# Kernel tuning notes

Hardware: AMD Instinct MI355X
Metric: run time of the kernel (lower is better)

The kernel has to match this reference:

```python
import jax, jax.numpy as jnp
import numpy as np

N = 50000          # num member nodes == num provider nodes
E = 800000         # provider->member bipartite edges (avg degree 16)
IN_M = 128; IN_P = 128; HID = 128; HEADS = 4; LAT = 64
NEG = 0.2          # leaky_relu negative slope (PyG GATConv default)


def gat_conv(x, src, dst, W, a_src, a_dst, b, heads, ch):
    """PyG-style GATConv (eval mode, concat heads). x:[N,F], src/dst:[Etot]."""
    n = x.shape[0]
    h = (x @ W).reshape(n, heads, ch)                       # [N,H,C]
    s = jnp.sum(h * a_src, axis=-1)                         # [N,H]
    d = jnp.sum(h * a_dst, axis=-1)                         # [N,H]
    e = jax.nn.leaky_relu(s[src] + d[dst], NEG)             # [Etot,H]
    # segment softmax over edges grouped by destination node
    m = jax.ops.segment_max(e, dst, num_segments=n)
    p = jnp.exp(e - m[dst])
    z = jax.ops.segment_sum(p, dst, num_segments=n)
    alpha = p / (z[dst] + 1e-16)                            # [Etot,H]
    out = jax.ops.segment_sum(h[src] * alpha[..., None], dst, num_segments=n)
    return out.reshape(n, heads * ch) + b


def setup_inputs() -> dict:
    key = jax.random.key(0)
    ks = jax.random.split(key, 24)
    gl = lambda k, shape, fan: (jax.random.normal(k, shape, jnp.float32) / np.sqrt(fan).astype(np.float32))
    return {
        "x_member": jax.random.normal(ks[0], (N, IN_M), jnp.float32),
        "x_provider": jax.random.normal(ks[1], (N, IN_P), jnp.float32),
        "edge_index": jax.random.randint(ks[2], (2, E), 0, N),
        "W1_m": gl(ks[3], (IN_M, HID), IN_M),
        "a_src1_m": gl(ks[4], (HEADS, HID // HEADS), HID // HEADS),
        "a_dst1_m": gl(ks[5], (HEADS, HID // HEADS), HID // HEADS),
        "b1_m": jnp.zeros((HID,), jnp.float32),
        "W2_m": gl(ks[6], (HID, LAT), HID),
        "a_src2_m": gl(ks[7], (1, LAT), LAT),
        "a_dst2_m": gl(ks[8], (1, LAT), LAT),
        "b2_m": jnp.zeros((LAT,), jnp.float32),
        "W1_p": gl(ks[9], (IN_P, HID), IN_P),
        "a_src1_p": gl(ks[10], (HEADS, HID // HEADS), HID // HEADS),
        "a_dst1_p": gl(ks[11], (HEADS, HID // HEADS), HID // HEADS),
        "b1_p": jnp.zeros((HID,), jnp.float32),
        "W2_p": gl(ks[12], (HID, LAT), HID),
        "a_src2_p": gl(ks[13], (1, LAT), LAT),
        "a_dst2_p": gl(ks[14], (1, LAT), LAT),
        "b2_p": jnp.zeros((LAT,), jnp.float32),
        "Wd_m": gl(ks[15], (LAT, IN_M), LAT),
        "bd_m": jnp.zeros((IN_M,), jnp.float32),
        "Wd_p": gl(ks[16], (LAT, IN_P), LAT),
        "bd_p": jnp.zeros((IN_P,), jnp.float32),
    }


def reference(x_member, x_provider, edge_index,
              W1_m, a_src1_m, a_dst1_m, b1_m, W2_m, a_src2_m, a_dst2_m, b2_m,
              W1_p, a_src1_p, a_dst1_p, b1_p, W2_p, a_src2_p, a_dst2_p, b2_p,
              Wd_m, bd_m, Wd_p, bd_p):
    prov, memb = edge_index[0], edge_index[1]
    loop = jnp.arange(N)
    # member graph: self loops + (provider -> member); provider graph: reverse
    m_src = jnp.concatenate([loop, prov]); m_dst = jnp.concatenate([loop, memb])
    p_src = jnp.concatenate([loop, memb]); p_dst = jnp.concatenate([loop, prov])

    xm = jax.nn.elu(gat_conv(x_member, m_src, m_dst, W1_m, a_src1_m, a_dst1_m, b1_m, HEADS, HID // HEADS))
    z_m = gat_conv(xm, m_src, m_dst, W2_m, a_src2_m, a_dst2_m, b2_m, 1, LAT)

    xp = jax.nn.elu(gat_conv(x_provider, p_src, p_dst, W1_p, a_src1_p, a_dst1_p, b1_p, HEADS, HID // HEADS))
    z_p = gat_conv(xp, p_src, p_dst, W2_p, a_src2_p, a_dst2_p, b2_p, 1, LAT)

    x_hat_member = z_m @ Wd_m + bd_m
    x_hat_provider = z_p @ Wd_p + bd_p
    edge_logits = jnp.sum(z_p[prov] * z_m[memb], axis=1)
    return (x_hat_member, x_hat_provider, edge_logits)
```

## Files before the change

kernel.cpp:

```cpp
#include <hip/hip_runtime.h>
#include <hip/hip_fp16.h>
#include <stdint.h>

__device__ __forceinline__ unsigned int pack_h2(float a, float b) {
    return (unsigned int)__half_as_ushort(__float2half(a)) |
           ((unsigned int)__half_as_ushort(__float2half(b)) << 16);
}
__device__ __forceinline__ float4 cvt_h4(uint2 r) {
    __half2 h0 = *reinterpret_cast<__half2*>(&r.x);
    __half2 h1 = *reinterpret_cast<__half2*>(&r.y);
    float2 f0 = __half22float2(h0), f1 = __half22float2(h1);
    return make_float4(f0.x, f0.y, f1.x, f1.y);
}

template<int K, int COUT, bool ADD_BIAS, bool IN_HALF, bool OUT_HALF, int SDH>
__global__ __launch_bounds__(256) void gemm_kernel(const void* __restrict__ X0,
                                                   const void* __restrict__ X1,
                                                   const float* __restrict__ W0,
                                                   const float* __restrict__ W1,
                                                   const float* __restrict__ b0,
                                                   const float* __restrict__ b1,
                                                   const float* __restrict__ as0,
                                                   const float* __restrict__ ad0,
                                                   const float* __restrict__ as1,
                                                   const float* __restrict__ ad1,
                                                   float* __restrict__ s_out,
                                                   float* __restrict__ d_out,
                                                   void* __restrict__ out0,
                                                   void* __restrict__ out1, int n)
{
    constexpr int KC   = 64;
    constexpr int CPT  = (COUT >= 128) ? 8 : 4;
    constexpr int TX   = COUT / CPT;
    constexpr int TY   = 256 / TX;
    constexpr int ROWS = TY * 4;

    __shared__ float Wl[KC * COUT];
    __shared__ float Xl[KC * ROWS];

    const int side = blockIdx.y;
    const void*  Xv   = side ? X1 : X0;
    const float* W    = side ? W1 : W0;
    const float* bias = side ? b1 : b0;
    void* outp        = side ? out1 : out0;

    const int tid  = threadIdx.x;
    const int row0 = blockIdx.x * ROWS;
    const int tx = tid % TX, ty = tid / TX;
    const int c0 = tx * CPT;

    float acc[4][CPT];
    #pragma unroll
    for (int i = 0; i < 4; ++i)
        #pragma unroll
        for (int j = 0; j < CPT; ++j) acc[i][j] = 0.f;

    for (int k0 = 0; k0 < K; k0 += KC) {
        for (int i = tid; i < KC * COUT / 4; i += 256) {
            int e0 = i * 4;
            int r = e0 / COUT, c = e0 - r * COUT;
            reinterpret_cast<float4*>(Wl)[i] =
                *reinterpret_cast<const float4*>(W + (size_t)(k0 + r) * COUT + c);
        }
        for (int i = tid; i < ROWS * KC / 4; i += 256) {
            int r = i / (KC / 4), c4 = i - r * (KC / 4);
            int gr = row0 + r;
            float4 v = make_float4(0.f, 0.f, 0.f, 0.f);
            if (gr < n) {
                if constexpr (IN_HALF) {
                    const __half* X = (const __half*)Xv;
                    v = cvt_h4(*reinterpret_cast<const uint2*>(X + (size_t)gr * K + k0 + c4 * 4));
                } else {
                    const float* X = (const float*)Xv;
                    v = *reinterpret_cast<const float4*>(X + (size_t)gr * K + k0 + c4 * 4);
                }
            }
            int cb = c4 * 4;
            Xl[(cb + 0) * ROWS + r] = v.x;
            Xl[(cb + 1) * ROWS + r] = v.y;
            Xl[(cb + 2) * ROWS + r] = v.z;
            Xl[(cb + 3) * ROWS + r] = v.w;
        }
        __syncthreads();

        #pragma unroll 16
        for (int kk = 0; kk < KC; ++kk) {
            float b[CPT];
            #pragma unroll
            for (int j = 0; j < CPT; ++j) b[j] = Wl[kk * COUT + c0 + j];
            float4 a4 = *reinterpret_cast<const float4*>(Xl + kk * ROWS + ty * 4);
            float a[4] = {a4.x, a4.y, a4.z, a4.w};
            #pragma unroll
            for (int i = 0; i < 4; ++i)
                #pragma unroll
                for (int j = 0; j < CPT; ++j)
                    acc[i][j] = fmaf(a[i], b[j], acc[i][j]);
        }
        __syncthreads();
    }

    float ascr[CPT], adtr[CPT];
    int hd = 0;
    if constexpr (SDH > 0) {
        constexpr int CHh = COUT / SDH;
        hd = c0 / CHh;
        const float* asc = (side ? as1 : as0) + c0;
        const float* adt = (side ? ad1 : ad0) + c0;
        #pragma unroll
        for (int j = 0; j < CPT; ++j) { ascr[j] = asc[j]; adtr[j] = adt[j]; }
    }

    #pragma unroll
    for (int i = 0; i < 4; ++i) {
        int gr = row0 + ty * 4 + i;
        if (gr < n) {
            float v[CPT];
            #pragma unroll
            for (int j = 0; j < CPT; ++j) {
                v[j] = acc[i][j];
                if constexpr (ADD_BIAS) v[j] += bias[c0 + j];
            }
            if constexpr (SDH > 0) {
                constexpr int CHh = COUT / SDH;
                constexpr int GL = CHh / CPT;
                float ps = 0.f, pd = 0.f;
                #pragma unroll
                for (int j = 0; j < CPT; ++j) {
                    ps = fmaf(v[j], ascr[j], ps);
                    pd = fmaf(v[j], adtr[j], pd);
                }
                #pragma unroll
                for (int o = 1; o < GL; o <<= 1) {
                    ps += __shfl_xor(ps, o, 64);
                    pd += __shfl_xor(pd, o, 64);
                }
                if ((tx % GL) == 0) {
                    size_t gi = (size_t)(side ? n + gr : gr) * SDH + hd;
                    s_out[gi] = ps; d_out[gi] = pd;
                }
            }
            if constexpr (OUT_HALF) {
                __half* po = (__half*)outp + (size_t)gr * COUT + c0;
                if constexpr (CPT == 8) {
                    uint4 w;
                    w.x = pack_h2(v[0], v[1]); w.y = pack_h2(v[2], v[3]);
                    w.z = pack_h2(v[4], v[5]); w.w = pack_h2(v[6], v[7]);
                    *reinterpret_cast<uint4*>(po) = w;
                } else {
                    uint2 w;
                    w.x = pack_h2(v[0], v[1]); w.y = pack_h2(v[2], v[3]);
                    *reinterpret_cast<uint2*>(po) = w;
                }
            } else {
                float* po = (float*)outp + (size_t)gr * COUT + c0;
                #pragma unroll
                for (int j = 0; j < CPT; ++j) po[j] = v[j];
            }
        }
    }
}

#define BSH 7
#define BCAP 2560
#define CHUNK_E 4096

__global__ __launch_bounds__(256) void bucket_scatter_kernel(const int* __restrict__ prov,
                                                             const int* __restrict__ memb,
                                                             int* __restrict__ bcnt,
                                                             int2* __restrict__ bstore,
                                                             int e, int n, int nbuck)
{
    __shared__ int hist[1024];
    __shared__ int lbase[1024];
    const int tid = threadIdx.x;
    const int e0 = blockIdx.x * CHUNK_E;
    const int e1 = min(e, e0 + CHUNK_E);

    for (int i = tid; i < nbuck; i += 256) hist[i] = 0;
    __syncthreads();
    for (int t = e0 + tid; t < e1; t += 256) {
        int m = memb[t], p = prov[t];
        atomicAdd(&hist[m >> BSH], 1);
        atomicAdd(&hist[(n + p) >> BSH], 1);
    }
    __syncthreads();
    for (int i = tid; i < nbuck; i += 256) {
        int h = hist[i];
        lbase[i] = (h > 0) ? atomicAdd(&bcnt[i], h) : 0;
        hist[i] = 0;
    }
    __syncthreads();
    for (int t = e0 + tid; t < e1; t += 256) {
        int m = memb[t], p = prov[t];
        int b1 = m >> BSH;
        int pos1 = lbase[b1] + atomicAdd(&hist[b1], 1);
        if (pos1 < BCAP) bstore[(size_t)b1 * BCAP + pos1] = make_int2(m, p);
        int d2 = n + p;
        int b2 = d2 >> BSH;
        int pos2 = lbase[b2] + atomicAdd(&hist[b2], 1);
        if (pos2 < BCAP) bstore[(size_t)b2 * BCAP + pos2] = make_int2(d2, m);
    }
}

__global__ __launch_bounds__(1024) void bucket_scan_kernel(const int* __restrict__ bcnt,
                                                           int* __restrict__ bbase,
                                                           int* __restrict__ roff,
                                                           int nb, int n2)
{
    __shared__ int tmp[1024];
    int tid = threadIdx.x;
    int v = (tid < nb) ? min(bcnt[tid], BCAP) : 0;
    tmp[tid] = v; __syncthreads();
    for (int o = 1; o < 1024; o <<= 1) {
        int x = (tid >= o) ? tmp[tid - o] : 0;
        __syncthreads();
        tmp[tid] += x;
        __syncthreads();
    }
    bbase[tid] = tmp[tid] - v;
    if (tid == 0) roff[n2] = tmp[1023];
}

__global__ __launch_bounds__(256) void bucket_build_kernel(const int* __restrict__ bcnt,
                                                           const int* __restrict__ bbase,
                                                           const int2* __restrict__ bstore,
                                                           int* __restrict__ roff,
                                                           int* __restrict__ colA,
                                                           int n2)
{
    __shared__ int2 ent[BCAP];
    __shared__ int  colL[BCAP];
    __shared__ int  cnts[128], pref[128], curs[128];

    const int b = blockIdx.x, tid = threadIdx.x;
    const int node0 = b << BSH;
    const int cnt  = min(bcnt[b], BCAP);
    const int base = bbase[b];

    if (tid < 128) cnts[tid] = 0;
    __syncthreads();
    for (int i = tid; i < cnt; i += 256) {
        int2 v = bstore[(size_t)b * BCAP + i];
        ent[i] = v;
        atomicAdd(&cnts[v.x - node0], 1);
    }
    __syncthreads();
    if (tid < 128) pref[tid] = cnts[tid];
    __syncthreads();
    #pragma unroll
    for (int o = 1; o < 128; o <<= 1) {
        int x = 0;
        if (tid < 128 && tid >= o) x = pref[tid - o];
        __syncthreads();
        if (tid < 128) pref[tid] += x;
        __syncthreads();
    }
    if (tid < 128) {
        int node = node0 + tid;
        if (node < n2) roff[node] = base + pref[tid] - cnts[tid];
        curs[tid] = 0;
    }
    __syncthreads();
    for (int i = tid; i < cnt; i += 256) {
        int2 v = ent[i];
        int loc = v.x - node0;
        int slot = (pref[loc] - cnts[loc]) + atomicAdd(&curs[loc], 1);
        colL[slot] = v.y;
    }
    __syncthreads();
    for (int i = tid; i < cnt; i += 256) colA[base + i] = colL[i];
}

template<int H>
__device__ __forceinline__ void store_alpha(__half* __restrict__ A, size_t e, const float* a) {
    if constexpr (H == 4) {
        uint2 w; w.x = pack_h2(a[0], a[1]); w.y = pack_h2(a[2], a[3]);
        *reinterpret_cast<uint2*>(A + e * 4) = w;
    } else {
        A[e] = __float2half(a[0]);
    }
}

template<int H>
__device__ __forceinline__ void alpha_one_fullwave(int iG, int lane,
                                                   const float* __restrict__ sarr,
                                                   const float* __restrict__ sb,
                                                   const float* __restrict__ darr,
                                                   const int* __restrict__ roff,
                                                   const int* __restrict__ col,
                                                   __half* __restrict__ A,
                                                   __half* __restrict__ aselfA)
{
    const int start = roff[iG], end = roff[iG + 1];
    const int deg = end - start;

    float dh[H], es[H];
    #pragma unroll
    for (int hh = 0; hh < H; ++hh) {
        dh[hh] = darr[(size_t)iG * H + hh];
        float e = sarr[(size_t)iG * H + hh] + dh[hh];
        es[hh] = fmaxf(e, 0.2f * e);
    }

    if (deg <= 64) {
        int srcL = (lane < deg) ? col[start + lane] : 0;
        float pl[H];
        if (lane < deg) {
            #pragma unroll
            for (int hh = 0; hh < H; ++hh) {
                float e = sb[(size_t)srcL * H + hh] + dh[hh];
                pl[hh] = __expf(fmaxf(e, 0.2f * e));
            }
        } else {
            #pragma unroll
            for (int hh = 0; hh < H; ++hh) pl[hh] = 0.f;
        }
        float zh[H];
        #pragma unroll
        for (int hh = 0; hh < H; ++hh) zh[hh] = pl[hh];
        #pragma unroll
        for (int hh = 0; hh < H; ++hh)
            for (int o = 32; o >= 1; o >>= 1)
                zh[hh] += __shfl_xor(zh[hh], o, 64);
        float av[H], sf[H];
        #pragma unroll
        for (int hh = 0; hh < H; ++hh) {
            float se = __expf(es[hh]);
            float invz = 1.f / (zh[hh] + se + 1e-16f);
            sf[hh] = se * invz;
            av[hh] = pl[hh] * invz;
        }
        if (lane < deg) store_alpha<H>(A, (size_t)(start + lane), av);
        if (lane == 0) store_alpha<H>(aselfA, (size_t)iG, sf);
        return;
    }

    float zh[H];
    #pragma unroll
    for (int hh = 0; hh < H; ++hh) zh[hh] = 0.f;
    for (int base = start; base < end; base += 64) {
        int idx = base + lane;
        if (idx < end) {
            int src = col[idx];
            #pragma unroll
            for (int hh = 0; hh < H; ++hh) {
                float e = sb[(size_t)src * H + hh] + dh[hh];
                e = fmaxf(e, 0.2f * e);
                zh[hh] += __expf(e);
            }
        }
    }
    #pragma unroll
    for (int hh = 0; hh < H; ++hh)
        for (int o = 32; o >= 1; o >>= 1)
            zh[hh] += __shfl_xor(zh[hh], o, 64);
    float invz[H], sf[H];
    #pragma unroll
    for (int hh = 0; hh < H; ++hh) {
        float se = __expf(es[hh]);
        invz[hh] = 1.f / (zh[hh] + se + 1e-16f);
        sf[hh] = se * invz[hh];
    }
    if (lane == 0) store_alpha<H>(aselfA, (size_t)iG, sf);
    for (int base = start; base < end; base += 64) {
        int idx = base + lane;
        if (idx < end) {
            int src = col[idx];
            float av[H];
            #pragma unroll
            for (int hh = 0; hh < H; ++hh) {
                float e = sb[(size_t)src * H + hh] + dh[hh];
                e = fmaxf(e, 0.2f * e);
                av[hh] = __expf(e) * invz[hh];
            }
            store_alpha<H>(A, (size_t)idx, av);
        }
    }
}

template<int H>
__global__ __launch_bounds__(256) void alpha_kernel(const float* __restrict__ sarr,
                                                    const float* __restrict__ darr,
                                                    const int* __restrict__ roff,
                                                    const int* __restrict__ col,
                                                    __half* __restrict__ A,
                                                    __half* __restrict__ aselfA, int N)
{
    const int n2 = 2 * N;
    const int lane = threadIdx.x & 63;
    const int g = lane >> 5, l = lane & 31;
    const int nw  = (gridDim.x * 256) >> 6;
    const int wv0 = (blockIdx.x * 256 + threadIdx.x) >> 6;
    const int npair = (n2 + 1) >> 1;

    for (int pr = wv0; pr < npair; pr += nw) {
        const int i0 = pr * 2;
        const bool nval = (i0 + g) < n2;
        const int iN = nval ? (i0 + g) : (n2 - 1);
        const int start = roff[iN], end = roff[iN + 1];
        const int deg = nval ? (end - start) : 0;
        const int degO = __shfl_xor(deg, 32, 64);

        if (max(deg, degO) <= 32) {
            const int side = (iN >= N) ? 1 : 0;
            const float* sb = sarr + (size_t)side * N * H;
            float dh[H], es[H];
            if constexpr (H == 4) {
                float4 dv = *reinterpret_cast<const float4*>(darr + (size_t)iN * 4);
                float4 sv = *reinterpret_cast<const float4*>(sarr + (size_t)iN * 4);
                dh[0] = dv.x; dh[1] = dv.y; dh[2] = dv.z; dh[3] = dv.w;
                float ev[4] = {sv.x + dv.x, sv.y + dv.y, sv.z + dv.z, sv.w + dv.w};
                #pragma unroll
                for (int hh = 0; hh < 4; ++hh) es[hh] = fmaxf(ev[hh], 0.2f * ev[hh]);
            } else {
                #pragma unroll
                for (int hh = 0; hh < H; ++hh) {
                    dh[hh] = darr[(size_t)iN * H + hh];
                    float e = sarr[(size_t)iN * H + hh] + dh[hh];
                    es[hh] = fmaxf(e, 0.2f * e);
                }
            }
            int srcL = (l < deg) ? col[start + l] : 0;
            float pl[H];
            if (l < deg) {
                if constexpr (H == 4) {
                    float4 sv = *reinterpret_cast<const float4*>(sb + (size_t)srcL * 4);
                    float ee[4] = {sv.x + dh[0], sv.y + dh[1], sv.z + dh[2], sv.w + dh[3]};
                    #pragma unroll
                    for (int hh = 0; hh < 4; ++hh) pl[hh] = __expf(fmaxf(ee[hh], 0.2f * ee[hh]));
                } else {
                    #pragma unroll
                    for (int hh = 0; hh < H; ++hh) {
                        float e = sb[(size_t)srcL * H + hh] + dh[hh];
                        pl[hh] = __expf(fmaxf(e, 0.2f * e));
                    }
                }
            } else {
                #pragma unroll
                for (int hh = 0; hh < H; ++hh) pl[hh] = 0.f;
            }
            float zh[H];
            #pragma unroll
            for (int hh = 0; hh < H; ++hh) zh[hh] = pl[hh];
            #pragma unroll
            for (int hh = 0; hh < H; ++hh)
                #pragma unroll
                for (int o = 16; o >= 1; o >>= 1)
                    zh[hh] += __shfl_xor(zh[hh], o, 64);
            float av[H], sf[H];
            #pragma unroll
            for (int hh = 0; hh < H; ++hh) {
                float se = __expf(es[hh]);
                float invz = 1.f / (zh[hh] + se + 1e-16f);
                sf[hh] = se * invz;
                av[hh] = pl[hh] * invz;
            }
            if (l < deg) store_alpha<H>(A, (size_t)(start + l), av);
            if (l == 0 && nval) store_alpha<H>(aselfA, (size_t)iN, sf);
        } else {
            for (int nd = 0; nd < 2; ++nd) {
                int i = i0 + nd;
                if (i >= n2) break;
                int sd2 = (i >= N) ? 1 : 0;
                alpha_one_fullwave<H>(i, lane, sarr, sarr + (size_t)sd2 * N * H, darr,
                                      roff, col, A, aselfA);
            }
        }
    }
}

template<int C, int H, bool ELU, bool OUTH>
__global__ __launch_bounds__(256) void gather_kernel(const __half* __restrict__ hm,
                                                     const __half* __restrict__ hp,
                                                     const __half* __restrict__ A,
                                                     const __half* __restrict__ aselfA,
                                                     const int* __restrict__ roff,
                                                     const int* __restrict__ col,
                                                     const float* __restrict__ bias_m,
                                                     const float* __restrict__ bias_p,
                                                     void* __restrict__ out_m,
                                                     void* __restrict__ out_p, int N)
{
    constexpr int CH  = C / H;
    constexpr int LRd = C / 8;
    constexpr int EPd = 32 / LRd;
    const int n2 = 2 * N;
    const int lane = threadIdx.x & 63;
    const int g = lane >> 5, l = lane & 31;
    const int sub = l / LRd, q = l % LRd;
    const int c0 = q * 8;
    const int hd = c0 / CH;
    const int nw  = (gridDim.x * 256) >> 6;
    const int wv0 = (blockIdx.x * 256 + threadIdx.x) >> 6;
    const int npair = (n2 + 1) >> 1;

    for (int pr = wv0; pr < npair; pr += nw) {
        const int i0 = pr * 2;
        const bool nval = (i0 + g) < n2;
        const int iN = nval ? (i0 + g) : (n2 - 1);
        const int side = (iN >= N) ? 1 : 0;
        const int lN = iN - side * N;
        const __half* hf = side ? hp : hm;
        const int start = roff[iN];
        const int deg = roff[iN + 1] - start;

        float acc[8];
        #pragma unroll
        for (int j = 0; j < 8; ++j) acc[j] = 0.f;
        if (sub == 0) {
            uint4 r = *reinterpret_cast<const uint4*>(hf + (size_t)lN * C + c0);
            float4 lo = cvt_h4(make_uint2(r.x, r.y));
            float4 hi = cvt_h4(make_uint2(r.z, r.w));
            float a = __half2float(aselfA[(size_t)iN * H + hd]);
            acc[0] = a * lo.x; acc[1] = a * lo.y; acc[2] = a * lo.z; acc[3] = a * lo.w;
            acc[4] = a * hi.x; acc[5] = a * hi.y; acc[6] = a * hi.z; acc[7] = a * hi.w;
        }
        int t = sub;
#define GSTEP(U)                                                                     \
        while (t + (U - 1) * EPd < deg) {                                            \
            int ss[U]; float aa[U]; uint4 rr[U];                                     \
            _Pragma("unroll")                                                        \
            for (int u = 0; u < U; ++u) {                                            \
                int e = start + t + u * EPd;                                         \
                ss[u] = col[e];                                                      \
                aa[u] = __half2float(A[(size_t)e * H + hd]);                         \
            }                                                                        \
            _Pragma("unroll")                                                        \
            for (int u = 0; u < U; ++u)                                              \
                rr[u] = *reinterpret_cast<const uint4*>(hf + (size_t)ss[u] * C + c0); \
            _Pragma("unroll")                                                        \
            for (int u = 0; u < U; ++u) {                                            \
                float4 lo = cvt_h4(make_uint2(rr[u].x, rr[u].y));                    \
                float4 hi = cvt_h4(make_uint2(rr[u].z, rr[u].w));                    \
                acc[0] = fmaf(aa[u], lo.x, acc[0]);                                  \
                acc[1] = fmaf(aa[u], lo.y, acc[1]);                                  \
                acc[2] = fmaf(aa[u], lo.z, acc[2]);                                  \
                acc[3] = fmaf(aa[u], lo.w, acc[3]);                                  \
                acc[4] = fmaf(aa[u], hi.x, acc[4]);                                  \
                acc[5] = fmaf(aa[u], hi.y, acc[5]);                                  \
                acc[6] = fmaf(aa[u], hi.z, acc[6]);                                  \
                acc[7] = fmaf(aa[u], hi.w, acc[7]);                                  \
            }                                                                        \
            t += U * EPd;                                                            \
        }
        GSTEP(4)
        GSTEP(2)
        GSTEP(1)
#undef GSTEP
        #pragma unroll
        for (int o = LRd; o < 32; o <<= 1) {
            #pragma unroll
            for (int j = 0; j < 8; ++j) acc[j] += __shfl_xor(acc[j], o, 64);
        }
        if (sub == 0 && nval) {
            const float* biasS = side ? bias_p : bias_m;
            float4 b0 = *reinterpret_cast<const float4*>(biasS + c0);
            float4 b1 = *reinterpret_cast<const float4*>(biasS + c0 + 4);
            float v[8] = {acc[0] + b0.x, acc[1] + b0.y, acc[2] + b0.z, acc[3] + b0.w,
                          acc[4] + b1.x, acc[5] + b1.y, acc[6] + b1.z, acc[7] + b1.w};
            if constexpr (ELU) {
                #pragma unroll
                for (int j = 0; j < 8; ++j) v[j] = (v[j] > 0.f) ? v[j] : (__expf(v[j]) - 1.f);
            }
            if constexpr (OUTH) {
                __half* outS = (__half*)(side ? out_p : out_m);
                uint4 w;
                w.x = pack_h2(v[0], v[1]); w.y = pack_h2(v[2], v[3]);
                w.z = pack_h2(v[4], v[5]); w.w = pack_h2(v[6], v[7]);
                *reinterpret_cast<uint4*>(outS + (size_t)lN * C + c0) = w;
            } else {
                float* outS = (float*)(side ? out_p : out_m);
                float* po = outS + (size_t)lN * C + c0;
                *reinterpret_cast<float4*>(po)     = make_float4(v[0], v[1], v[2], v[3]);
                *reinterpret_cast<float4*>(po + 4) = make_float4(v[4], v[5], v[6], v[7]);
            }
        }
    }
}

__global__ __launch_bounds__(256) void logits_kernel(const __half* __restrict__ zp,
                                                     const __half* __restrict__ zm,
                                                     const int* __restrict__ prov,
                                                     const int* __restrict__ memb,
                                                     float* __restrict__ outv, int e)
{
    const int nw   = (gridDim.x * 256) >> 6;
    const int wv   = (blockIdx.x * 256 + threadIdx.x) >> 6;
    const int lane = threadIdx.x & 63;
    const int g = lane >> 3, q = lane & 7;
    const int c0 = q * 8;
    for (int base = wv * 16; base < e; base += nw * 16) {
        int e1 = base + g, e2 = base + 8 + g;
        bool v1 = e1 < e, v2 = e2 < e;
        int i1 = v1 ? e1 : (e - 1), i2 = v2 ? e2 : (e - 1);
        int p1 = prov[i1], m1 = memb[i1];
        int p2 = prov[i2], m2 = memb[i2];
        uint4 a1 = *reinterpret_cast<const uint4*>(zp + (size_t)p1 * 64 + c0);
        uint4 b1 = *reinterpret_cast<const uint4*>(zm + (size_t)m1 * 64 + c0);
        uint4 a2 = *reinterpret_cast<const uint4*>(zp + (size_t)p2 * 64 + c0);
        uint4 b2 = *reinterpret_cast<const uint4*>(zm + (size_t)m2 * 64 + c0);
        float4 al1 = cvt_h4(make_uint2(a1.x, a1.y)), ah1 = cvt_h4(make_uint2(a1.z, a1.w));
        float4 bl1 = cvt_h4(make_uint2(b1.x, b1.y)), bh1 = cvt_h4(make_uint2(b1.z, b1.w));
        float4 al2 = cvt_h4(make_uint2(a2.x, a2.y)), ah2 = cvt_h4(make_uint2(a2.z, a2.w));
        float4 bl2 = cvt_h4(make_uint2(b2.x, b2.y)), bh2 = cvt_h4(make_uint2(b2.z, b2.w));
        float s1 = al1.x * bl1.x + al1.y * bl1.y + al1.z * bl1.z + al1.w * bl1.w
                 + ah1.x * bh1.x + ah1.y * bh1.y + ah1.z * bh1.z + ah1.w * bh1.w;
        float s2 = al2.x * bl2.x + al2.y * bl2.y + al2.z * bl2.z + al2.w * bl2.w
                 + ah2.x * bh2.x + ah2.y * bh2.y + ah2.z * bh2.z + ah2.w * bh2.w;
        #pragma unroll
        for (int o = 1; o < 8; o <<= 1) {
            s1 += __shfl_xor(s1, o, 64);
            s2 += __shfl_xor(s2, o, 64);
        }
        if (q == 0) {
            if (v1) outv[e1] = s1;
            if (v2) outv[e2] = s2;
        }
    }
}

extern "C" void kernel_launch(void* const* d_in, const int* in_sizes, int n_in,
                              void* d_out, int out_size, void* d_ws, size_t ws_size,
                              hipStream_t stream)
{
    const int N_ = in_sizes[0] / 128;
    const int E_ = in_sizes[2] / 2;

    const float* x_member   = (const float*)d_in[0];
    const float* x_provider = (const float*)d_in[1];
    const int*   prov = (const int*)d_in[2];
    const int*   memb = prov + E_;
    const float* W1_m = (const float*)d_in[3];
    const float* a_src1_m = (const float*)d_in[4];
    const float* a_dst1_m = (const float*)d_in[5];
    const float* b1_m = (const float*)d_in[6];
    const float* W2_m = (const float*)d_in[7];
    const float* a_src2_m = (const float*)d_in[8];
    const float* a_dst2_m = (const float*)d_in[9];
    const float* b2_m = (const float*)d_in[10];
    const float* W1_p = (const float*)d_in[11];
    const float* a_src1_p = (const float*)d_in[12];
    const float* a_dst1_p = (const float*)d_in[13];
    const float* b1_p = (const float*)d_in[14];
    const float* W2_p = (const float*)d_in[15];
    const float* a_src2_p = (const float*)d_in[16];
    const float* a_dst2_p = (const float*)d_in[17];
    const float* b2_p = (const float*)d_in[18];
    const float* Wd_m = (const float*)d_in[19];
    const float* bd_m = (const float*)d_in[20];
    const float* Wd_p = (const float*)d_in[21];
    const float* bd_p = (const float*)d_in[22];

    const int n2 = 2 * N_;
    const int NB = (n2 + 127) >> BSH;

    char* p = (char*)d_ws;
    auto alloc = [&](size_t bytes) { void* q = (void*)p; p += (bytes + 255) & ~(size_t)255; return q; };
    __half* h1m   = (__half*)alloc((size_t)N_ * 128 * 2);
    __half* h1p   = (__half*)alloc((size_t)N_ * 128 * 2);
    __half* xm16m = (__half*)alloc((size_t)N_ * 128 * 2);
    __half* xm16p = (__half*)alloc((size_t)N_ * 128 * 2);
    __half* zm16  = (__half*)alloc((size_t)N_ * 64 * 2);
    __half* zp16  = (__half*)alloc((size_t)N_ * 64 * 2);
    float* s1     = (float*)alloc((size_t)n2 * 4 * 4);
    float* d1     = (float*)alloc((size_t)n2 * 4 * 4);
    __half* alpha2= (__half*)alloc((size_t)2 * E_ * 2);
    __half* aselfH= (__half*)alloc((size_t)n2 * 4 * 2);
    int*   bcnt   = (int*)alloc((size_t)NB * 4);
    int*   bbase  = (int*)alloc(1024 * 4);
    int*   roff2  = (int*)alloc((size_t)(n2 + 1) * 4);
    int*   colA   = (int*)alloc((size_t)2 * E_ * 4);
    __half* h2m = h1m;
    __half* h2p = h1p;
    int2*  bstore = (int2*)h1m;
    __half* alpha1 = zm16;

    hipMemsetAsync(bcnt, 0, (size_t)NB * 4, stream);
    bucket_scatter_kernel<<<(E_ + CHUNK_E - 1) / CHUNK_E, 256, 0, stream>>>(prov, memb, bcnt, bstore, E_, N_, NB);
    bucket_scan_kernel<<<1, 1024, 0, stream>>>(bcnt, bbase, roff2, NB, n2);
    bucket_build_kernel<<<NB, 256, 0, stream>>>(bcnt, bbase, bstore, roff2, colA, n2);

    const dim3 gg((N_ + 63) / 64, 2);
    float* out = (float*)d_out;

    gemm_kernel<128, 128, false, false, true, 4><<<gg, 256, 0, stream>>>(
        x_member, x_provider, W1_m, W1_p, nullptr, nullptr,
        a_src1_m, a_dst1_m, a_src1_p, a_dst1_p, s1, d1, h1m, h1p, N_);
    alpha_kernel<4><<<2048, 256, 0, stream>>>(s1, d1, roff2, colA, alpha1, aselfH, N_);
    gather_kernel<128, 4, true, true><<<2048, 256, 0, stream>>>(
        h1m, h1p, alpha1, aselfH, roff2, colA, b1_m, b1_p, xm16m, xm16p, N_);

    gemm_kernel<128, 64, false, true, true, 1><<<gg, 256, 0, stream>>>(
        xm16m, xm16p, W2_m, W2_p, nullptr, nullptr,
        a_src2_m, a_dst2_m, a_src2_p, a_dst2_p, s1, d1, h2m, h2p, N_);
    alpha_kernel<1><<<2048, 256, 0, stream>>>(s1, d1, roff2, colA, alpha2, aselfH, N_);
    gather_kernel<64, 1, false, true><<<2048, 256, 0, stream>>>(
        h2m, h2p, alpha2, aselfH, roff2, colA, b2_m, b2_p, zm16, zp16, N_);

    gemm_kernel<64, 128, true, true, false, 0><<<gg, 256, 0, stream>>>(
        zm16, zp16, Wd_m, Wd_p, bd_m, bd_p,
        nullptr, nullptr, nullptr, nullptr, nullptr, nullptr,
        out, out + (size_t)N_ * 128, N_);
    logits_kernel<<<2048, 256, 0, stream>>>(zp16, zm16, prov, memb, out + (size_t)N_ * 128 * 2, E_);
}
```

Measured before the change: 474.3 us.

## Restructure GEMM shared-memory layout to avoid bank conflicts and interleave column groups

Rewrites the dense GEMM tile so each thread owns two interleaved 4-column groups, 64 columns apart, instead of 8 contiguous columns. The X tile stride is padded by one to reduce LDS bank conflicts on the transposed stores. The K chunk is halved to 32 and the load loops are unrolled. The attention-score reduction is rewritten per head layout to match the new column mapping. The padded stride stops the A reads from being float4-aligned, so they become scalar LDS loads. Smaller K chunks also double the number of syncs.

```diff
diff --git a/kernel.cpp b/kernel.cpp
--- a/kernel.cpp
+++ b/kernel.cpp
@@ -29,14 +29,15 @@
                                                    void* __restrict__ out0,
                                                    void* __restrict__ out1, int n)
 {
-    constexpr int KC   = 64;
-    constexpr int CPT  = (COUT >= 128) ? 8 : 4;
-    constexpr int TX   = COUT / CPT;
+    constexpr int KC   = 32;
+    constexpr int NG   = (COUT >= 128) ? 2 : 1;
+    constexpr int TX   = COUT / (4 * NG);
     constexpr int TY   = 256 / TX;
     constexpr int ROWS = TY * 4;
+    constexpr int XS   = ROWS + 1;
 
     __shared__ float Wl[KC * COUT];
-    __shared__ float Xl[KC * ROWS];
+    __shared__ float Xl[KC * XS];
 
     const int side = blockIdx.y;
     const void*  Xv   = side ? X1 : X0;
@@ -47,21 +48,24 @@
     const int tid  = threadIdx.x;
     const int row0 = blockIdx.x * ROWS;
     const int tx = tid % TX, ty = tid / TX;
-    const int c0 = tx * CPT;
-
-    float acc[4][CPT];
+
+    float acc[4][NG][4];
     #pragma unroll
     for (int i = 0; i < 4; ++i)
         #pragma unroll
-        for (int j = 0; j < CPT; ++j) acc[i][j] = 0.f;
+        for (int g = 0; g < NG; ++g)
+            #pragma unroll
+            for (int j = 0; j < 4; ++j) acc[i][g][j] = 0.f;
 
     for (int k0 = 0; k0 < K; k0 += KC) {
+        #pragma unroll
         for (int i = tid; i < KC * COUT / 4; i += 256) {
             int e0 = i * 4;
             int r = e0 / COUT, c = e0 - r * COUT;
             reinterpret_cast<float4*>(Wl)[i] =
                 *reinterpret_cast<const float4*>(W + (size_t)(k0 + r) * COUT + c);
         }
+        #pragma unroll
         for (int i = tid; i < ROWS * KC / 4; i += 256) {
             int r = i / (KC / 4), c4 = i - r * (KC / 4);
             int gr = row0 + r;
@@ -76,85 +80,112 @@
                 }
             }
             int cb = c4 * 4;
-            Xl[(cb + 0) * ROWS + r] = v.x;
-            Xl[(cb + 1) * ROWS + r] = v.y;
-            Xl[(cb + 2) * ROWS + r] = v.z;
-            Xl[(cb + 3) * ROWS + r] = v.w;
+            Xl[(cb + 0) * XS + r] = v.x;
+            Xl[(cb + 1) * XS + r] = v.y;
+            Xl[(cb + 2) * XS + r] = v.z;
+            Xl[(cb + 3) * XS + r] = v.w;
         }
         __syncthreads();
 
         #pragma unroll 16
         for (int kk = 0; kk < KC; ++kk) {
-            float b[CPT];
-            #pragma unroll
-            for (int j = 0; j < CPT; ++j) b[j] = Wl[kk * COUT + c0 + j];
-            float4 a4 = *reinterpret_cast<const float4*>(Xl + kk * ROWS + ty * 4);
-            float a[4] = {a4.x, a4.y, a4.z, a4.w};
+            float4 b[NG];
+            #pragma unroll
+            for (int g = 0; g < NG; ++g)
+                b[g] = *reinterpret_cast<const float4*>(Wl + kk * COUT + g * 64 + tx * 4);
+            const float* xp = Xl + kk * XS + ty * 4;
+            float a[4] = {xp[0], xp[1], xp[2], xp[3]};
             #pragma unroll
             for (int i = 0; i < 4; ++i)
                 #pragma unroll
-                for (int j = 0; j < CPT; ++j)
-                    acc[i][j] = fmaf(a[i], b[j], acc[i][j]);
+                for (int g = 0; g < NG; ++g) {
+                    acc[i][g][0] = fmaf(a[i], b[g].x, acc[i][g][0]);
+                    acc[i][g][1] = fmaf(a[i], b[g].y, acc[i][g][1]);
+                    acc[i][g][2] = fmaf(a[i], b[g].z, acc[i][g][2]);
+                    acc[i][g][3] = fmaf(a[i], b[g].w, acc[i][g][3]);
+                }
         }
         __syncthreads();
     }
 
-    float ascr[CPT], adtr[CPT];
-    int hd = 0;
+    float ascr[NG][4], adtr[NG][4];
     if constexpr (SDH > 0) {
-        constexpr int CHh = COUT / SDH;
-        hd = c0 / CHh;
-        const float* asc = (side ? as1 : as0) + c0;
-        const float* adt = (side ? ad1 : ad0) + c0;
-        #pragma unroll
-        for (int j = 0; j < CPT; ++j) { ascr[j] = asc[j]; adtr[j] = adt[j]; }
+        const float* asc = side ? as1 : as0;
+        const float* adt = side ? ad1 : ad0;
+        #pragma unroll
+        for (int g = 0; g < NG; ++g)
+            #pragma unroll
+            for (int j = 0; j < 4; ++j) {
+                ascr[g][j] = asc[g * 64 + tx * 4 + j];
+                adtr[g][j] = adt[g * 64 + tx * 4 + j];
+            }
     }
 
     #pragma unroll
     for (int i = 0; i < 4; ++i) {
         int gr = row0 + ty * 4 + i;
         if (gr < n) {
-            float v[CPT];
-            #pragma unroll
-            for (int j = 0; j < CPT; ++j) {
-                v[j] = acc[i][j];
-                if constexpr (ADD_BIAS) v[j] += bias[c0 + j];
-            }
-            if constexpr (SDH > 0) {
-                constexpr int CHh = COUT / SDH;
-                constexpr int GL = CHh / CPT;
-                float ps = 0.f, pd = 0.f;
-                #pragma unroll
-                for (int j = 0; j < CPT; ++j) {
-                    ps = fmaf(v[j], ascr[j], ps);
-                    pd = fmaf(v[j], adtr[j], pd);
-                }
-                #pragma unroll
-                for (int o = 1; o < GL; o <<= 1) {
-                    ps += __shfl_xor(ps, o, 64);
-                    pd += __shfl_xor(pd, o, 64);
-                }
-                if ((tx % GL) == 0) {
-                    size_t gi = (size_t)(side ? n + gr : gr) * SDH + hd;
-                    s_out[gi] = ps; d_out[gi] = pd;
-                }
-            }
-            if constexpr (OUT_HALF) {
-                __half* po = (__half*)outp + (size_t)gr * COUT + c0;
-                if constexpr (CPT == 8) {
-                    uint4 w;
-                    w.x = pack_h2(v[0], v[1]); w.y = pack_h2(v[2], v[3]);
-                    w.z = pack_h2(v[4], v[5]); w.w = pack_h2(v[6], v[7]);
-                    *reinterpret_cast<uint4*>(po) = w;
+            float v[NG][4];
+            #pragma unroll
+            for (int g = 0; g < NG; ++g)
+                #pragma unroll
+                for (int j = 0; j < 4; ++j) {
+                    v[g][j] = acc[i][g][j];
+                    if constexpr (ADD_BIAS) v[g][j] += bias[g * 64 + tx * 4 + j];
+                }
+            if constexpr (SDH == 4) {
+                float ps[2], pd[2];
+                #pragma unroll
+                for (int g = 0; g < 2; ++g) {
+                    float s = 0.f, d = 0.f;
+                    #pragma unroll
+                    for (int j = 0; j < 4; ++j) {
+                        s = fmaf(v[g][j], ascr[g][j], s);
+                        d = fmaf(v[g][j], adtr[g][j], d);
+                    }
+                    ps[g] = s; pd[g] = d;
+                }
+                #pragma unroll
+                for (int o = 1; o < 8; o <<= 1) {
+                    #pragma unroll
+                    for (int g = 0; g < 2; ++g) {
+                        ps[g] += __shfl_xor(ps[g], o, 64);
+                        pd[g] += __shfl_xor(pd[g], o, 64);
+                    }
+                }
+                if ((tx & 7) == 0) {
+                    size_t gi = (size_t)(side ? n + gr : gr) * 4 + (tx >> 3);
+                    s_out[gi] = ps[0];     d_out[gi] = pd[0];
+                    s_out[gi + 2] = ps[1]; d_out[gi + 2] = pd[1];
+                }
+            } else if constexpr (SDH == 1) {
+                float s = 0.f, d = 0.f;
+                #pragma unroll
+                for (int j = 0; j < 4; ++j) {
+                    s = fmaf(v[0][j], ascr[0][j], s);
+                    d = fmaf(v[0][j], adtr[0][j], d);
+                }
+                #pragma unroll
+                for (int o = 1; o < 16; o <<= 1) {
+                    s += __shfl_xor(s, o, 64);
+                    d += __shfl_xor(d, o, 64);
+                }
+                if (tx == 0) {
+                    size_t gi = (size_t)(side ? n + gr : gr);
+                    s_out[gi] = s; d_out[gi] = d;
+                }
+            }
+            #pragma unroll
+            for (int g = 0; g < NG; ++g) {
+                if constexpr (OUT_HALF) {
+                    __half* po = (__half*)outp + (size_t)gr * COUT + g * 64 + tx * 4;
+                    uint2 w;
+                    w.x = pack_h2(v[g][0], v[g][1]); w.y = pack_h2(v[g][2], v[g][3]);
+                    *reinterpret_cast<uint2*>(po) = w;
                 } else {
-                    uint2 w;
-                    w.x = pack_h2(v[0], v[1]); w.y = pack_h2(v[2], v[3]);
-                    *reinterpret_cast<uint2*>(po) = w;
-                }
-            } else {
-                float* po = (float*)outp + (size_t)gr * COUT + c0;
-                #pragma unroll
-                for (int j = 0; j < CPT; ++j) po[j] = v[j];
+                    float* po = (float*)outp + (size_t)gr * COUT + g * 64 + tx * 4;
+                    *reinterpret_cast<float4*>(po) = make_float4(v[g][0], v[g][1], v[g][2], v[g][3]);
+                }
             }
         }
     }
```

New measurement: 446.5 us. 1.06x faster.

## Replace FP32 SIMT GEMMs with MFMA f16 GEMMs and fold attention vectors into weights

Applied to the files above, without the earlier changes.

Swaps the shared-memory FP32 FMA GEMM for a wave-level MFMA 16x16x32 f16 kernel that reads operands directly from global memory. A small prep kernel converts each weight matrix to a transposed f16 layout and appends extra columns holding W·a_src and W·a_dst, so the per-node attention scores come out of the same MFMA pass instead of a shuffle reduction. This targets the ALU-bound dense projections. In exchange, the first-layer input and the weights are rounded to f16 before multiplication, which adds rounding error, and the output stores become scalar and strided per lane.

```diff
diff --git a/kernel.cpp b/kernel.cpp
--- a/kernel.cpp
+++ b/kernel.cpp
@@ -1,6 +1,10 @@
 #include <hip/hip_runtime.h>
 #include <hip/hip_fp16.h>
 #include <stdint.h>
+
+typedef _Float16 f16_t;
+typedef _Float16 f16x8 __attribute__((ext_vector_type(8)));
+typedef float f32x4 __attribute__((ext_vector_type(4)));
 
 __device__ __forceinline__ unsigned int pack_h2(float a, float b) {
     return (unsigned int)__half_as_ushort(__float2half(a)) |
@@ -13,148 +17,124 @@
     return make_float4(f0.x, f0.y, f1.x, f1.y);
 }
 
-template<int K, int COUT, bool ADD_BIAS, bool IN_HALF, bool OUT_HALF, int SDH>
-__global__ __launch_bounds__(256) void gemm_kernel(const void* __restrict__ X0,
-                                                   const void* __restrict__ X1,
-                                                   const float* __restrict__ W0,
-                                                   const float* __restrict__ W1,
-                                                   const float* __restrict__ b0,
-                                                   const float* __restrict__ b1,
-                                                   const float* __restrict__ as0,
-                                                   const float* __restrict__ ad0,
-                                                   const float* __restrict__ as1,
-                                                   const float* __restrict__ ad1,
-                                                   float* __restrict__ s_out,
-                                                   float* __restrict__ d_out,
-                                                   void* __restrict__ out0,
-                                                   void* __restrict__ out1, int n)
-{
-    constexpr int KC   = 64;
-    constexpr int CPT  = (COUT >= 128) ? 8 : 4;
-    constexpr int TX   = COUT / CPT;
-    constexpr int TY   = 256 / TX;
-    constexpr int ROWS = TY * 4;
-
-    __shared__ float Wl[KC * COUT];
-    __shared__ float Xl[KC * ROWS];
+__global__ __launch_bounds__(256) void prep_kernel(
+    const float* __restrict__ W1m, const float* __restrict__ as1m, const float* __restrict__ ad1m,
+    const float* __restrict__ W1p, const float* __restrict__ as1p, const float* __restrict__ ad1p,
+    const float* __restrict__ W2m, const float* __restrict__ as2m, const float* __restrict__ ad2m,
+    const float* __restrict__ W2p, const float* __restrict__ as2p, const float* __restrict__ ad2p,
+    const float* __restrict__ Wdm, const float* __restrict__ Wdp,
+    f16_t* __restrict__ B1m, f16_t* __restrict__ B1p,
+    f16_t* __restrict__ B2m, f16_t* __restrict__ B2p,
+    f16_t* __restrict__ Bdm, f16_t* __restrict__ Bdp)
+{
+    const float *W = nullptr, *as = nullptr, *ad = nullptr;
+    f16_t* B = nullptr; int K = 0, COUT = 0, H = 0;
+    switch (blockIdx.x) {
+        case 0: W = W1m; as = as1m; ad = ad1m; B = B1m; K = 128; COUT = 128; H = 4; break;
+        case 1: W = W1p; as = as1p; ad = ad1p; B = B1p; K = 128; COUT = 128; H = 4; break;
+        case 2: W = W2m; as = as2m; ad = ad2m; B = B2m; K = 128; COUT = 64;  H = 1; break;
+        case 3: W = W2p; as = as2p; ad = ad2p; B = B2p; K = 128; COUT = 64;  H = 1; break;
+        case 4: W = Wdm; B = Bdm; K = 64; COUT = 128; H = 0; break;
+        case 5: W = Wdp; B = Bdp; K = 64; COUT = 128; H = 0; break;
+    }
+    const int total = (COUT + 16) * K;
+    for (int idx = threadIdx.x; idx < total; idx += 256) {
+        int c = idx / K, k = idx - c * K;
+        float v = 0.f;
+        if (c < COUT) {
+            v = W[(size_t)k * COUT + c];
+        } else {
+            int e = c - COUT;
+            if (H > 0 && e < 2 * H) {
+                int h = (e < H) ? e : e - H;
+                const float* av = (e < H) ? as : ad;
+                int CH = COUT / H;
+                for (int cc = 0; cc < CH; ++cc)
+                    v += W[(size_t)k * COUT + h * CH + cc] * av[h * CH + cc];
+            }
+        }
+        B[idx] = (f16_t)v;
+    }
+}
+
+template<int K, int COUT, bool IN_HALF, bool OUT_HALF, int SDH, bool ADD_BIAS>
+__global__ __launch_bounds__(256) void mfma_gemm(const void* __restrict__ X0,
+                                                 const void* __restrict__ X1,
+                                                 const f16_t* __restrict__ B0,
+                                                 const f16_t* __restrict__ B1,
+                                                 const float* __restrict__ b0,
+                                                 const float* __restrict__ b1,
+                                                 float* __restrict__ s_out,
+                                                 float* __restrict__ d_out,
+                                                 void* __restrict__ out0,
+                                                 void* __restrict__ out1, int n)
+{
+    constexpr int NT = COUT / 16;
+    constexpr int TT = NT + ((SDH > 0) ? 1 : 0);
 
     const int side = blockIdx.y;
-    const void*  Xv   = side ? X1 : X0;
-    const float* W    = side ? W1 : W0;
+    const void*  Xv = side ? X1 : X0;
+    const f16_t* B  = side ? B1 : B0;
     const float* bias = side ? b1 : b0;
-    void* outp        = side ? out1 : out0;
-
-    const int tid  = threadIdx.x;
-    const int row0 = blockIdx.x * ROWS;
-    const int tx = tid % TX, ty = tid / TX;
-    const int c0 = tx * CPT;
-
-    float acc[4][CPT];
-    #pragma unroll
-    for (int i = 0; i < 4; ++i)
-        #pragma unroll
-        for (int j = 0; j < CPT; ++j) acc[i][j] = 0.f;
-
-    for (int k0 = 0; k0 < K; k0 += KC) {
-        for (int i = tid; i < KC * COUT / 4; i += 256) {
-            int e0 = i * 4;
-            int r = e0 / COUT, c = e0 - r * COUT;
-            reinterpret_cast<float4*>(Wl)[i] =
-                *reinterpret_cast<const float4*>(W + (size_t)(k0 + r) * COUT + c);
-        }
-        for (int i = tid; i < ROWS * KC / 4; i += 256) {
-            int r = i / (KC / 4), c4 = i - r * (KC / 4);
-            int gr = row0 + r;
-            float4 v = make_float4(0.f, 0.f, 0.f, 0.f);
-            if (gr < n) {
-                if constexpr (IN_HALF) {
-                    const __half* X = (const __half*)Xv;
-                    v = cvt_h4(*reinterpret_cast<const uint2*>(X + (size_t)gr * K + k0 + c4 * 4));
-                } else {
-                    const float* X = (const float*)Xv;
-                    v = *reinterpret_cast<const float4*>(X + (size_t)gr * K + k0 + c4 * 4);
-                }
-            }
-            int cb = c4 * 4;
-            Xl[(cb + 0) * ROWS + r] = v.x;
-            Xl[(cb + 1) * ROWS + r] = v.y;
-            Xl[(cb + 2) * ROWS + r] = v.z;
-            Xl[(cb + 3) * ROWS + r] = v.w;
-        }
-        __syncthreads();
-
-        #pragma unroll 16
-        for (int kk = 0; kk < KC; ++kk) {
-            float b[CPT];
-            #pragma unroll
-            for (int j = 0; j < CPT; ++j) b[j] = Wl[kk * COUT + c0 + j];
-            float4 a4 = *reinterpret_cast<const float4*>(Xl + kk * ROWS + ty * 4);
-            float a[4] = {a4.x, a4.y, a4.z, a4.w};
-            #pragma unroll
-            for (int i = 0; i < 4; ++i)
-                #pragma unroll
-                for (int j = 0; j < CPT; ++j)
-                    acc[i][j] = fmaf(a[i], b[j], acc[i][j]);
-        }
-        __syncthreads();
-    }
-
-    float ascr[CPT], adtr[CPT];
-    int hd = 0;
+    void* outp = side ? out1 : out0;
+
+    const int wid  = threadIdx.x >> 6;
+    const int lane = threadIdx.x & 63;
+    const int r0 = blockIdx.x * 64 + wid * 16;
+    if (r0 >= n) return;
+    const int col = lane & 15;
+    const int kg  = lane >> 4;
+    const int arow = min(r0 + col, n - 1);
+
+    f32x4 acc[TT];
+    #pragma unroll
+    for (int t = 0; t < TT; ++t) acc[t] = (f32x4)0.f;
+
+    #pragma unroll
+    for (int kb = 0; kb < K; kb += 32) {
+        f16x8 a;
+        if constexpr (IN_HALF) {
+            a = *reinterpret_cast<const f16x8*>((const f16_t*)Xv + (size_t)arow * K + kb + kg * 8);
+        } else {
+            const float* xp = (const float*)Xv + (size_t)arow * K + kb + kg * 8;
+            float4 u = *reinterpret_cast<const float4*>(xp);
+            float4 w = *reinterpret_cast<const float4*>(xp + 4);
+            a[0] = (f16_t)u.x; a[1] = (f16_t)u.y; a[2] = (f16_t)u.z; a[3] = (f16_t)u.w;
+            a[4] = (f16_t)w.x; a[5] = (f16_t)w.y; a[6] = (f16_t)w.z; a[7] = (f16_t)w.w;
+        }
+        #pragma unroll
+        for (int t = 0; t < TT; ++t) {
+            f16x8 bf = *reinterpret_cast<const f16x8*>(B + (size_t)(t * 16 + col) * K + kb + kg * 8);
+            acc[t] = __builtin_amdgcn_mfma_f32_16x16x32_f16(a, bf, acc[t], 0, 0, 0);
+        }
+    }
+
+    const int rb = r0 + 4 * (lane >> 4);
+    #pragma unroll
+    for (int t = 0; t < NT; ++t) {
+        float bv = 0.f;
+        if constexpr (ADD_BIAS) bv = bias[t * 16 + col];
+        #pragma unroll
+        for (int j = 0; j < 4; ++j) {
+            int row = rb + j;
+            if (row < n) {
+                float v = acc[t][j] + bv;
+                if constexpr (OUT_HALF)
+                    ((__half*)outp)[(size_t)row * COUT + t * 16 + col] = __float2half(v);
+                else
+                    ((float*)outp)[(size_t)row * COUT + t * 16 + col] = v;
+            }
+        }
+    }
     if constexpr (SDH > 0) {
-        constexpr int CHh = COUT / SDH;
-        hd = c0 / CHh;
-        const float* asc = (side ? as1 : as0) + c0;
-        const float* adt = (side ? ad1 : ad0) + c0;
-        #pragma unroll
-        for (int j = 0; j < CPT; ++j) { ascr[j] = asc[j]; adtr[j] = adt[j]; }
-    }
-
-    #pragma unroll
-    for (int i = 0; i < 4; ++i) {
-        int gr = row0 + ty * 4 + i;
-        if (gr < n) {
-            float v[CPT];
-            #pragma unroll
-            for (int j = 0; j < CPT; ++j) {
-                v[j] = acc[i][j];
-                if constexpr (ADD_BIAS) v[j] += bias[c0 + j];
-            }
-            if constexpr (SDH > 0) {
-                constexpr int CHh = COUT / SDH;
-                constexpr int GL = CHh / CPT;
-                float ps = 0.f, pd = 0.f;
-                #pragma unroll
-                for (int j = 0; j < CPT; ++j) {
-                    ps = fmaf(v[j], ascr[j], ps);
-                    pd = fmaf(v[j], adtr[j], pd);
-                }
-                #pragma unroll
-                for (int o = 1; o < GL; o <<= 1) {
-                    ps += __shfl_xor(ps, o, 64);
-                    pd += __shfl_xor(pd, o, 64);
-                }
-                if ((tx % GL) == 0) {
-                    size_t gi = (size_t)(side ? n + gr : gr) * SDH + hd;
-                    s_out[gi] = ps; d_out[gi] = pd;
-                }
-            }
-            if constexpr (OUT_HALF) {
-                __half* po = (__half*)outp + (size_t)gr * COUT + c0;
-                if constexpr (CPT == 8) {
-                    uint4 w;
-                    w.x = pack_h2(v[0], v[1]); w.y = pack_h2(v[2], v[3]);
-                    w.z = pack_h2(v[4], v[5]); w.w = pack_h2(v[6], v[7]);
-                    *reinterpret_cast<uint4*>(po) = w;
-                } else {
-                    uint2 w;
-                    w.x = pack_h2(v[0], v[1]); w.y = pack_h2(v[2], v[3]);
-                    *reinterpret_cast<uint2*>(po) = w;
-                }
-            } else {
-                float* po = (float*)outp + (size_t)gr * COUT + c0;
-                #pragma unroll
-                for (int j = 0; j < CPT; ++j) po[j] = v[j];
+        #pragma unroll
+        for (int j = 0; j < 4; ++j) {
+            int row = rb + j;
+            if (row < n) {
+                float v = acc[NT][j];
+                size_t gi = (size_t)(side ? n + row : row) * SDH;
+                if (col < SDH) s_out[gi + col] = v;
+                else if (col < 2 * SDH) d_out[gi + (col - SDH)] = v;
             }
         }
     }
@@ -670,6 +650,12 @@
     int*   bbase  = (int*)alloc(1024 * 4);
     int*   roff2  = (int*)alloc((size_t)(n2 + 1) * 4);
     int*   colA   = (int*)alloc((size_t)2 * E_ * 4);
+    f16_t* B1m = (f16_t*)alloc((size_t)(128 + 16) * 128 * 2);
+    f16_t* B1p = (f16_t*)alloc((size_t)(128 + 16) * 128 * 2);
+    f16_t* B2m = (f16_t*)alloc((size_t)(64 + 16) * 128 * 2);
+    f16_t* B2p = (f16_t*)alloc((size_t)(64 + 16) * 128 * 2);
+    f16_t* Bdm = (f16_t*)alloc((size_t)(128 + 16) * 64 * 2);
+    f16_t* Bdp = (f16_t*)alloc((size_t)(128 + 16) * 64 * 2);
     __half* h2m = h1m;
     __half* h2p = h1p;
     int2*  bstore = (int2*)h1m;
@@ -680,26 +666,28 @@
     bucket_scan_kernel<<<1, 1024, 0, stream>>>(bcnt, bbase, roff2, NB, n2);
     bucket_build_kernel<<<NB, 256, 0, stream>>>(bcnt, bbase, bstore, roff2, colA, n2);
 
+    prep_kernel<<<6, 256, 0, stream>>>(
+        W1_m, a_src1_m, a_dst1_m, W1_p, a_src1_p, a_dst1_p,
+        W2_m, a_src2_m, a_dst2_m, W2_p, a_src2_p, a_dst2_p,
+        Wd_m, Wd_p, B1m, B1p, B2m, B2p, Bdm, Bdp);
+
     const dim3 gg((N_ + 63) / 64, 2);
     float* out = (float*)d_out;
 
-    gemm_kernel<128, 128, false, false, true, 4><<<gg, 256, 0, stream>>>(
-        x_member, x_provider, W1_m, W1_p, nullptr, nullptr,
-        a_src1_m, a_dst1_m, a_src1_p, a_dst1_p, s1, d1, h1m, h1p, N_);
+    mfma_gemm<128, 128, false, true, 4, false><<<gg, 256, 0, stream>>>(
+        x_member, x_provider, B1m, B1p, nullptr, nullptr, s1, d1, h1m, h1p, N_);
     alpha_kernel<4><<<2048, 256, 0, stream>>>(s1, d1, roff2, colA, alpha1, aselfH, N_);
     gather_kernel<128, 4, true, true><<<2048, 256, 0, stream>>>(
         h1m, h1p, alpha1, aselfH, roff2, colA, b1_m, b1_p, xm16m, xm16p, N_);
 
-    gemm_kernel<128, 64, false, true, true, 1><<<gg, 256, 0, stream>>>(
-        xm16m, xm16p, W2_m, W2_p, nullptr, nullptr,
-        a_src2_m, a_dst2_m, a_src2_p, a_dst2_p, s1, d1, h2m, h2p, N_);
+    mfma_gemm<128, 64, true, true, 1, false><<<gg, 256, 0, stream>>>(
+        xm16m, xm16p, B2m, B2p, nullptr, nullptr, s1, d1, h2m, h2p, N_);
     alpha_kernel<1><<<2048, 256, 0, stream>>>(s1, d1, roff2, colA, alpha2, aselfH, N_);
     gather_kernel<64, 1, false, true><<<2048, 256, 0, stream>>>(
         h2m, h2p, alpha2, aselfH, roff2, colA, b2_m, b2_p, zm16, zp16, N_);
 
-    gemm_kernel<64, 128, true, true, false, 0><<<gg, 256, 0, stream>>>(
-        zm16, zp16, Wd_m, Wd_p, bd_m, bd_p,
-        nullptr, nullptr, nullptr, nullptr, nullptr, nullptr,
+    mfma_gemm<64, 128, true, false, 0, true><<<gg, 256, 0, stream>>>(
+        zm16, zp16, Bdm, Bdp, bd_m, bd_p, nullptr, nullptr,
         out, out + (size_t)N_ * 128, N_);
     logits_kernel<<<2048, 256, 0, stream>>>(zp16, zm16, prov, memb, out + (size_t)N_ * 128 * 2, E_);
 }
```

New measurement: 455.9 us. 1.04x faster.
